# Kernel tuning notes

Hardware: AMD Instinct MI355X
Metric: run time of the kernel (lower is better)

The kernel has to match this reference:

```python
import jax, jax.numpy as jnp
import numpy as np

N = 4096      # num nodes
FIN = 256     # num_in_features
H = 8         # num_of_heads
F = 64        # num_out_features per head
NEG = -1e9    # additive mask value for non-edges


def setup_inputs() -> dict:
    key = jax.random.key(0)
    ks = jax.random.split(key, 7)
    x = jax.random.normal(ks[0], (N, FIN), dtype=jnp.float32)
    adj = jax.random.bernoulli(ks[1], 0.01, (N, N)) | jnp.eye(N, dtype=bool)
    connectivity_mask = jnp.where(adj, 0.0, NEG).astype(jnp.float32)
    # Xavier-uniform-ish scaled params
    W = jax.random.normal(ks[2], (H * F, FIN), dtype=jnp.float32) * np.float32(1.0 / np.sqrt(FIN))
    a_src = jax.random.normal(ks[3], (1, H, F), dtype=jnp.float32) * np.float32(0.1)
    a_tgt = jax.random.normal(ks[4], (1, H, F), dtype=jnp.float32) * np.float32(0.1)
    skip_W = jax.random.normal(ks[5], (H * F, FIN), dtype=jnp.float32) * np.float32(1.0 / np.sqrt(FIN))
    bias = jnp.zeros((H * F,), dtype=jnp.float32)
    return {"x": x, "connectivity_mask": connectivity_mask, "W": W,
            "a_src": a_src, "a_tgt": a_tgt, "skip_W": skip_W, "bias": bias}


def reference(x, connectivity_mask, W, a_src, a_tgt, skip_W, bias):
    # linear_proj (no bias), view to [N, H, F]   (dropout omitted: eval mode)
    proj = (x @ W.T).reshape(N, H, F)
    # per-head scalar scores: [N, H] -> [H, N, 1] and [H, 1, N]
    s_src = jnp.sum(proj * a_src, axis=-1).T[:, :, None]   # [H, N, 1]
    s_tgt = jnp.sum(proj * a_tgt, axis=-1).T[:, None, :]   # [H, 1, N]
    scores = jax.nn.leaky_relu(s_src + s_tgt, negative_slope=0.2)  # [H, N, N]
    alpha = jax.nn.softmax(scores + connectivity_mask[None, :, :], axis=-1)
    # weighted aggregation: bmm(alpha, proj^T) then permute back to [N, H, F]
    out = jnp.einsum('hij,jhf->ihf', alpha, proj)
    # skip connection (dims differ: F_in=256 vs H*F output per head) -> skip_proj
    out = out + (x @ skip_W.T).reshape(N, H, F)
    # concat heads, add bias, ELU activation
    out = out.reshape(N, H * F) + bias
    return jax.nn.elu(out)
```

## Files before the change

### kernel.cpp

```cpp
#include <hip/hip_runtime.h>
#include <hip/hip_bf16.h>

#define NN 4096
#define FIN 256
#define NH 8
#define NF 64
#define HF 512
#define MAXD 128

typedef __attribute__((ext_vector_type(4))) float f32x4;
typedef __attribute__((ext_vector_type(8))) short short8;
typedef unsigned short u16;
typedef unsigned int u32;

union Frag { uint4 u; short8 s; };

__device__ __forceinline__ u16 f2bf(float x) {
    u32 u = __float_as_uint(x);
    u += 0x7fffu + ((u >> 16) & 1u);
    return (u16)(u >> 16);
}
__device__ __forceinline__ float bf2f(u32 lo16) {
    return __uint_as_float(lo16 << 16);
}

__global__ __launch_bounds__(256) void cvt_kernel(
    const float* __restrict__ x, const float* __restrict__ W,
    const float* __restrict__ skW,
    u16* __restrict__ xh, u16* __restrict__ Wh, u16* __restrict__ skWh)
{
    const int gid = blockIdx.x * 256 + threadIdx.x;
    const float* src; u16* dst; int off;
    if (gid < 131072)      { src = x;   dst = xh;   off = gid; }
    else if (gid < 147456) { src = W;   dst = Wh;   off = gid - 131072; }
    else                   { src = skW; dst = skWh; off = gid - 147456; }
    const int e = off * 8;
    const float4 a = *(const float4*)&src[e];
    const float4 b = *(const float4*)&src[e + 4];
    union { u16 h[8]; uint4 v; } pk;
    pk.h[0]=f2bf(a.x); pk.h[1]=f2bf(a.y); pk.h[2]=f2bf(a.z); pk.h[3]=f2bf(a.w);
    pk.h[4]=f2bf(b.x); pk.h[5]=f2bf(b.y); pk.h[6]=f2bf(b.z); pk.h[7]=f2bf(b.w);
    *(uint4*)&dst[e] = pk.v;
}

__global__ __launch_bounds__(256) void gemm_mfma(
    const u16* __restrict__ xh, const u16* __restrict__ Wh,
    const u16* __restrict__ skWh,
    u16* __restrict__ projh, float* __restrict__ skipv)
{
    const int z = blockIdx.z;
    const u16* Bg = z ? skWh : Wh;
    const int bm = blockIdx.y * 128, bn = blockIdx.x * 128;
    __shared__ u16 lds[2][2][8192];
    const int t = threadIdx.x;
    const int w = t >> 6, lane = t & 63;
    const int wm = w >> 1, wn = w & 1;
    const int l15 = lane & 15, lk = lane >> 4;

    f32x4 acc[4][4] = {};

    auto stage = [&](int buf, int ks) {
        const int k0 = ks * 64;
        #pragma unroll
        for (int q = 0; q < 4; ++q) {
            const int s = q * 256 + t;
            const int kk = s >> 9, fr = (s >> 6) & 7;
            const int row = bm + fr * 16 + l15;
            const int kel = k0 + kk * 32 + lk * 8;
            u16* ldst = &lds[buf][0][(q * 256 + w * 64) * 8];
            __builtin_amdgcn_global_load_lds(
                (const __attribute__((address_space(1))) u32*)&xh[row * FIN + kel],
                (__attribute__((address_space(3))) u32*)ldst, 16, 0, 0);
        }
        #pragma unroll
        for (int q = 0; q < 4; ++q) {
            const int s = q * 256 + t;
            const int kk = s >> 9, fr = (s >> 6) & 7;
            const int row = bn + fr * 16 + l15;
            const int kel = k0 + kk * 32 + lk * 8;
            u16* ldst = &lds[buf][1][(q * 256 + w * 64) * 8];
            __builtin_amdgcn_global_load_lds(
                (const __attribute__((address_space(1))) u32*)&Bg[row * FIN + kel],
                (__attribute__((address_space(3))) u32*)ldst, 16, 0, 0);
        }
    };
    auto compute = [&](int buf) {
        const uint4* Ab = (const uint4*)&lds[buf][0][0];
        const uint4* Bb = (const uint4*)&lds[buf][1][0];
        #pragma unroll
        for (int kk = 0; kk < 2; ++kk) {
            Frag a[4], b[4];
            #pragma unroll
            for (int m = 0; m < 4; ++m) a[m].u = Ab[(kk * 8 + wm * 4 + m) * 64 + lane];
            #pragma unroll
            for (int n = 0; n < 4; ++n) b[n].u = Bb[(kk * 8 + wn * 4 + n) * 64 + lane];
            #pragma unroll
            for (int m = 0; m < 4; ++m)
                #pragma unroll
                for (int n = 0; n < 4; ++n)
                    acc[m][n] = __builtin_amdgcn_mfma_f32_16x16x32_bf16(
                        a[m].s, b[n].s, acc[m][n], 0, 0, 0);
        }
    };

    stage(0, 0);
    asm volatile("s_waitcnt vmcnt(0)" ::: "memory");
    __syncthreads();
    int buf = 0;
    for (int ks = 0; ks < 4; ++ks) {
        if (ks < 3) stage(buf ^ 1, ks + 1);
        compute(buf);
        asm volatile("s_waitcnt vmcnt(0)" ::: "memory");
        __syncthreads();
        buf ^= 1;
    }

    #pragma unroll
    for (int m = 0; m < 4; ++m) {
        const int r0 = bm + wm * 64 + m * 16 + lk * 4;
        #pragma unroll
        for (int n = 0; n < 4; ++n) {
            const int c = bn + wn * 64 + n * 16 + l15;
            if (z == 0) {
                #pragma unroll
                for (int rr = 0; rr < 4; ++rr)
                    projh[(size_t)(r0 + rr) * HF + c] = f2bf(acc[m][n][rr]);
            } else {
                #pragma unroll
                for (int rr = 0; rr < 4; ++rr)
                    skipv[(size_t)(r0 + rr) * HF + c] = acc[m][n][rr];
            }
        }
    }
}

__global__ __launch_bounds__(256) void s_kernel(
    const u16* __restrict__ projh, const float* __restrict__ a_src,
    const float* __restrict__ a_tgt, float* __restrict__ s_src,
    float* __restrict__ s_tgt)
{
    const int wg = (blockIdx.x * 256 + threadIdx.x) >> 6;
    const int lane = threadIdx.x & 63;
    const int i = wg >> 3, h = wg & 7;
    const float v = bf2f(projh[(size_t)i * HF + h * NF + lane]);
    float ps = v * a_src[h * NF + lane];
    float pt = v * a_tgt[h * NF + lane];
    #pragma unroll
    for (int off = 32; off; off >>= 1) {
        ps += __shfl_xor(ps, off);
        pt += __shfl_xor(pt, off);
    }
    if (lane == 0) { s_src[h * NN + i] = ps; s_tgt[h * NN + i] = pt; }
}

__global__ __launch_bounds__(256) void scan_kernel(
    const float* __restrict__ mask, int* __restrict__ cnt_g,
    int* __restrict__ nbr_g)
{
    const int i = blockIdx.x, t = threadIdx.x;
    __shared__ int nbr_s[MAXD];
    __shared__ int cnt_s;
    if (t == 0) cnt_s = 0;
    __syncthreads();
    const float4* mrow = (const float4*)&mask[(size_t)i * NN];
    #pragma unroll
    for (int it = 0; it < 4; ++it) {
        const float4 v = mrow[it * 256 + t];
        const int j0 = (it * 256 + t) * 4;
        if (v.x > -0.5f) { int p = atomicAdd(&cnt_s, 1); if (p < MAXD) nbr_s[p] = j0; }
        if (v.y > -0.5f) { int p = atomicAdd(&cnt_s, 1); if (p < MAXD) nbr_s[p] = j0 + 1; }
        if (v.z > -0.5f) { int p = atomicAdd(&cnt_s, 1); if (p < MAXD) nbr_s[p] = j0 + 2; }
        if (v.w > -0.5f) { int p = atomicAdd(&cnt_s, 1); if (p < MAXD) nbr_s[p] = j0 + 3; }
    }
    __syncthreads();
    const int cnt = min(cnt_s, MAXD);
    if (t == 0) cnt_g[i] = cnt;
    if (t < cnt) nbr_g[i * MAXD + t] = nbr_s[t];
}

__global__ __launch_bounds__(256) void agg_kernel(
    const u16* __restrict__ projh, const int* __restrict__ cnt_g,
    const int* __restrict__ nbr_g,
    const float* __restrict__ s_src, const float* __restrict__ s_tgt,
    const float* __restrict__ skipv, const float* __restrict__ bias,
    float* __restrict__ out)
{
    const int i = blockIdx.x, t = threadIdx.x;
    __shared__ int nbr_s[MAXD + 8];
    __shared__ float alpha_s[NH][MAXD + 8];
    __shared__ int cnt_sh;
    if (t == 0) cnt_sh = cnt_g[i];
    __syncthreads();
    const int cnt = cnt_sh;
    if (t < cnt) nbr_s[t] = nbr_g[i * MAXD + t];
    if (t < 8) nbr_s[cnt + t] = i;
    __syncthreads();

    {
        const int h = t >> 5, l = t & 31;
        const float ss = s_src[h * NN + i];
        float sc[4]; float m = -1e30f;
        #pragma unroll
        for (int q = 0; q < 4; ++q) {
            const int k = l + 32 * q;
            if (k < cnt) {
                float s = ss + s_tgt[h * NN + nbr_s[k]];
                s = s > 0.f ? s : 0.2f * s;
                sc[q] = s; m = fmaxf(m, s);
            } else sc[q] = -1e30f;
        }
        #pragma unroll
        for (int off = 16; off; off >>= 1) m = fmaxf(m, __shfl_xor(m, off));
        float p[4]; float psum = 0.f;
        #pragma unroll
        for (int q = 0; q < 4; ++q) {
            p[q] = exp2f((sc[q] - m) * 1.4426950408889634f);
            psum += p[q];
        }
        #pragma unroll
        for (int off = 16; off; off >>= 1) psum += __shfl_xor(psum, off);
        const float inv = 1.0f / psum;
        #pragma unroll
        for (int q = 0; q < 4; ++q) {
            const int k = l + 32 * q;
            if (k < cnt) alpha_s[h][k] = p[q] * inv;
        }
        if (l < 8) alpha_s[h][cnt + l] = 0.f;
    }
    __syncthreads();

    const int w = t >> 6, lane = t & 63;
    const int c = w * 128 + lane * 2;
    const int head = c >> 6, cidx = c >> 1;
    const u32* ph = (const u32*)projh;
    float acc0 = 0.f, acc1 = 0.f;
    const int kmax = (cnt + 7) & ~7;
    for (int k0 = 0; k0 < kmax; k0 += 8) {
        u32 v[8]; float av[8];
        #pragma unroll
        for (int u = 0; u < 8; ++u) {
            v[u] = ph[(size_t)nbr_s[k0 + u] * 256 + cidx];
            av[u] = alpha_s[head][k0 + u];
        }
        #pragma unroll
        for (int u = 0; u < 8; ++u) {
            acc0 += av[u] * bf2f(v[u] & 0xffffu);
            acc1 += av[u] * __uint_as_float(v[u] & 0xffff0000u);
        }
    }

    const float2 sk = *(const float2*)&skipv[(size_t)i * HF + c];
    const float2 bs = *(const float2*)&bias[c];
    float o0 = acc0 + sk.x + bs.x;
    float o1 = acc1 + sk.y + bs.y;
    o0 = o0 > 0.f ? o0 : expm1f(o0);
    o1 = o1 > 0.f ? o1 : expm1f(o1);
    *(float2*)&out[(size_t)i * HF + c] = make_float2(o0, o1);
}

extern "C" void kernel_launch(void* const* d_in, const int* in_sizes, int n_in,
                              void* d_out, int out_size, void* d_ws, size_t ws_size,
                              hipStream_t stream)
{
    (void)in_sizes; (void)n_in; (void)out_size; (void)ws_size;
    const float* x     = (const float*)d_in[0];
    const float* mask  = (const float*)d_in[1];
    const float* W     = (const float*)d_in[2];
    const float* a_src = (const float*)d_in[3];
    const float* a_tgt = (const float*)d_in[4];
    const float* skW   = (const float*)d_in[5];
    const float* bias  = (const float*)d_in[6];
    float* out = (float*)d_out;

    char* ws = (char*)d_ws;
    u16*   xh    = (u16*)(ws);
    u16*   Wh    = (u16*)(ws + 0x200000);
    u16*   skWh  = (u16*)(ws + 0x240000);
    u16*   projh = (u16*)(ws + 0x400000);
    float* skipv = (float*)(ws + 0x800000);
    float* s_src = (float*)(ws + 0x1000000);
    float* s_tgt = (float*)(ws + 0x1020000);
    int*   cnt_g = (int*)(ws + 0x1040000);
    int*   nbr_g = (int*)(ws + 0x1048000);

    scan_kernel<<<dim3(4096), 256, 0, stream>>>(mask, cnt_g, nbr_g);
    cvt_kernel<<<dim3(640), 256, 0, stream>>>(x, W, skW, xh, Wh, skWh);
    gemm_mfma<<<dim3(4, 32, 2), 256, 0, stream>>>(xh, Wh, skWh, projh, skipv);
    s_kernel<<<dim3(8192), 256, 0, stream>>>(projh, a_src, a_tgt, s_src, s_tgt);
    agg_kernel<<<dim3(4096), 256, 0, stream>>>(projh, cnt_g, nbr_g,
                                               s_src, s_tgt, skipv, bias, out);
}
```

Baseline: 145.4 us.

## Fuse scan with bf16 conversion and attention scores into GEMM epilogue

Merges the mask-scan and fp32-to-bf16 conversion kernels into one launch by splitting block ranges, and computes per-head source and target scores inside the projection GEMM epilogue from fp32 accumulators instead of a separate pass over bf16 proj. The score arrays are transposed to node-major layout so agg reads the 8 head scores per node contiguously. This removes two kernel launches and one full reread of proj. The scores now come from unrounded fp32 accumulators, so values change slightly.

```diff
diff --git a/kernel.cpp b/kernel.cpp
--- a/kernel.cpp
+++ b/kernel.cpp
@@ -24,29 +24,56 @@
     return __uint_as_float(lo16 << 16);
 }
 
-__global__ __launch_bounds__(256) void cvt_kernel(
+__global__ __launch_bounds__(256) void scan_cvt(
+    const float* __restrict__ mask, int* __restrict__ cnt_g,
+    int* __restrict__ nbr_g,
     const float* __restrict__ x, const float* __restrict__ W,
     const float* __restrict__ skW,
     u16* __restrict__ xh, u16* __restrict__ Wh, u16* __restrict__ skWh)
 {
-    const int gid = blockIdx.x * 256 + threadIdx.x;
-    const float* src; u16* dst; int off;
-    if (gid < 131072)      { src = x;   dst = xh;   off = gid; }
-    else if (gid < 147456) { src = W;   dst = Wh;   off = gid - 131072; }
-    else                   { src = skW; dst = skWh; off = gid - 147456; }
-    const int e = off * 8;
-    const float4 a = *(const float4*)&src[e];
-    const float4 b = *(const float4*)&src[e + 4];
-    union { u16 h[8]; uint4 v; } pk;
-    pk.h[0]=f2bf(a.x); pk.h[1]=f2bf(a.y); pk.h[2]=f2bf(a.z); pk.h[3]=f2bf(a.w);
-    pk.h[4]=f2bf(b.x); pk.h[5]=f2bf(b.y); pk.h[6]=f2bf(b.z); pk.h[7]=f2bf(b.w);
-    *(uint4*)&dst[e] = pk.v;
-}
-
-__global__ __launch_bounds__(256) void gemm_mfma(
+    const int t = threadIdx.x;
+    if (blockIdx.x >= 4096) {
+        const int gid = (blockIdx.x - 4096) * 256 + t;
+        const float* src; u16* dst; int off;
+        if (gid < 131072)      { src = x;   dst = xh;   off = gid; }
+        else if (gid < 147456) { src = W;   dst = Wh;   off = gid - 131072; }
+        else                   { src = skW; dst = skWh; off = gid - 147456; }
+        const int e = off * 8;
+        const float4 a = *(const float4*)&src[e];
+        const float4 b = *(const float4*)&src[e + 4];
+        union { u16 h[8]; uint4 v; } pk;
+        pk.h[0]=f2bf(a.x); pk.h[1]=f2bf(a.y); pk.h[2]=f2bf(a.z); pk.h[3]=f2bf(a.w);
+        pk.h[4]=f2bf(b.x); pk.h[5]=f2bf(b.y); pk.h[6]=f2bf(b.z); pk.h[7]=f2bf(b.w);
+        *(uint4*)&dst[e] = pk.v;
+        return;
+    }
+    const int i = blockIdx.x;
+    __shared__ int nbr_s[MAXD];
+    __shared__ int cnt_s;
+    if (t == 0) cnt_s = 0;
+    __syncthreads();
+    const float4* mrow = (const float4*)&mask[(size_t)i * NN];
+    #pragma unroll
+    for (int it = 0; it < 4; ++it) {
+        const float4 v = mrow[it * 256 + t];
+        const int j0 = (it * 256 + t) * 4;
+        if (v.x > -0.5f) { int p = atomicAdd(&cnt_s, 1); if (p < MAXD) nbr_s[p] = j0; }
+        if (v.y > -0.5f) { int p = atomicAdd(&cnt_s, 1); if (p < MAXD) nbr_s[p] = j0 + 1; }
+        if (v.z > -0.5f) { int p = atomicAdd(&cnt_s, 1); if (p < MAXD) nbr_s[p] = j0 + 2; }
+        if (v.w > -0.5f) { int p = atomicAdd(&cnt_s, 1); if (p < MAXD) nbr_s[p] = j0 + 3; }
+    }
+    __syncthreads();
+    const int cnt = min(cnt_s, MAXD);
+    if (t == 0) cnt_g[i] = cnt;
+    if (t < cnt) nbr_g[i * MAXD + t] = nbr_s[t];
+}
+
+__global__ __launch_bounds__(256) void gemm_s(
     const u16* __restrict__ xh, const u16* __restrict__ Wh,
     const u16* __restrict__ skWh,
-    u16* __restrict__ projh, float* __restrict__ skipv)
+    const float* __restrict__ a_src, const float* __restrict__ a_tgt,
+    u16* __restrict__ projh, float* __restrict__ skipv,
+    float* __restrict__ s_srcT, float* __restrict__ s_tgtT)
 {
     const int z = blockIdx.z;
     const u16* Bg = z ? skWh : Wh;
@@ -115,17 +142,54 @@
         buf ^= 1;
     }
 
-    #pragma unroll
-    for (int m = 0; m < 4; ++m) {
-        const int r0 = bm + wm * 64 + m * 16 + lk * 4;
-        #pragma unroll
-        for (int n = 0; n < 4; ++n) {
-            const int c = bn + wn * 64 + n * 16 + l15;
-            if (z == 0) {
+    if (z == 0) {
+        #pragma unroll
+        for (int m = 0; m < 4; ++m) {
+            const int r0 = bm + wm * 64 + m * 16 + lk * 4;
+            #pragma unroll
+            for (int n = 0; n < 4; ++n) {
+                const int c = bn + wn * 64 + n * 16 + l15;
                 #pragma unroll
                 for (int rr = 0; rr < 4; ++rr)
                     projh[(size_t)(r0 + rr) * HF + c] = f2bf(acc[m][n][rr]);
-            } else {
+            }
+        }
+        const int h = blockIdx.x * 2 + wn;
+        float as[4], at[4];
+        #pragma unroll
+        for (int n = 0; n < 4; ++n) {
+            as[n] = a_src[h * NF + n * 16 + l15];
+            at[n] = a_tgt[h * NF + n * 16 + l15];
+        }
+        #pragma unroll
+        for (int m = 0; m < 4; ++m) {
+            #pragma unroll
+            for (int rr = 0; rr < 4; ++rr) {
+                float ps = 0.f, pt = 0.f;
+                #pragma unroll
+                for (int n = 0; n < 4; ++n) {
+                    ps += acc[m][n][rr] * as[n];
+                    pt += acc[m][n][rr] * at[n];
+                }
+                #pragma unroll
+                for (int off = 8; off; off >>= 1) {
+                    ps += __shfl_xor(ps, off);
+                    pt += __shfl_xor(pt, off);
+                }
+                if (l15 == 0) {
+                    const int row = bm + wm * 64 + m * 16 + lk * 4 + rr;
+                    s_srcT[row * NH + h] = ps;
+                    s_tgtT[row * NH + h] = pt;
+                }
+            }
+        }
+    } else {
+        #pragma unroll
+        for (int m = 0; m < 4; ++m) {
+            const int r0 = bm + wm * 64 + m * 16 + lk * 4;
+            #pragma unroll
+            for (int n = 0; n < 4; ++n) {
+                const int c = bn + wn * 64 + n * 16 + l15;
                 #pragma unroll
                 for (int rr = 0; rr < 4; ++rr)
                     skipv[(size_t)(r0 + rr) * HF + c] = acc[m][n][rr];
@@ -134,54 +198,10 @@
     }
 }
 
-__global__ __launch_bounds__(256) void s_kernel(
-    const u16* __restrict__ projh, const float* __restrict__ a_src,
-    const float* __restrict__ a_tgt, float* __restrict__ s_src,
-    float* __restrict__ s_tgt)
-{
-    const int wg = (blockIdx.x * 256 + threadIdx.x) >> 6;
-    const int lane = threadIdx.x & 63;
-    const int i = wg >> 3, h = wg & 7;
-    const float v = bf2f(projh[(size_t)i * HF + h * NF + lane]);
-    float ps = v * a_src[h * NF + lane];
-    float pt = v * a_tgt[h * NF + lane];
-    #pragma unroll
-    for (int off = 32; off; off >>= 1) {
-        ps += __shfl_xor(ps, off);
-        pt += __shfl_xor(pt, off);
-    }
-    if (lane == 0) { s_src[h * NN + i] = ps; s_tgt[h * NN + i] = pt; }
-}
-
-__global__ __launch_bounds__(256) void scan_kernel(
-    const float* __restrict__ mask, int* __restrict__ cnt_g,
-    int* __restrict__ nbr_g)
-{
-    const int i = blockIdx.x, t = threadIdx.x;
-    __shared__ int nbr_s[MAXD];
-    __shared__ int cnt_s;
-    if (t == 0) cnt_s = 0;
-    __syncthreads();
-    const float4* mrow = (const float4*)&mask[(size_t)i * NN];
-    #pragma unroll
-    for (int it = 0; it < 4; ++it) {
-        const float4 v = mrow[it * 256 + t];
-        const int j0 = (it * 256 + t) * 4;
-        if (v.x > -0.5f) { int p = atomicAdd(&cnt_s, 1); if (p < MAXD) nbr_s[p] = j0; }
-        if (v.y > -0.5f) { int p = atomicAdd(&cnt_s, 1); if (p < MAXD) nbr_s[p] = j0 + 1; }
-        if (v.z > -0.5f) { int p = atomicAdd(&cnt_s, 1); if (p < MAXD) nbr_s[p] = j0 + 2; }
-        if (v.w > -0.5f) { int p = atomicAdd(&cnt_s, 1); if (p < MAXD) nbr_s[p] = j0 + 3; }
-    }
-    __syncthreads();
-    const int cnt = min(cnt_s, MAXD);
-    if (t == 0) cnt_g[i] = cnt;
-    if (t < cnt) nbr_g[i * MAXD + t] = nbr_s[t];
-}
-
 __global__ __launch_bounds__(256) void agg_kernel(
     const u16* __restrict__ projh, const int* __restrict__ cnt_g,
     const int* __restrict__ nbr_g,
-    const float* __restrict__ s_src, const float* __restrict__ s_tgt,
+    const float* __restrict__ s_srcT, const float* __restrict__ s_tgtT,
     const float* __restrict__ skipv, const float* __restrict__ bias,
     float* __restrict__ out)
 {
@@ -198,13 +218,13 @@
 
     {
         const int h = t >> 5, l = t & 31;
-        const float ss = s_src[h * NN + i];
+        const float ss = s_srcT[i * NH + h];
         float sc[4]; float m = -1e30f;
         #pragma unroll
         for (int q = 0; q < 4; ++q) {
             const int k = l + 32 * q;
             if (k < cnt) {
-                float s = ss + s_tgt[h * NN + nbr_s[k]];
+                float s = ss + s_tgtT[nbr_s[k] * NH + h];
                 s = s > 0.f ? s : 0.2f * s;
                 sc[q] = s; m = fmaxf(m, s);
             } else sc[q] = -1e30f;
@@ -273,20 +293,20 @@
     float* out = (float*)d_out;
 
     char* ws = (char*)d_ws;
-    u16*   xh    = (u16*)(ws);
-    u16*   Wh    = (u16*)(ws + 0x200000);
-    u16*   skWh  = (u16*)(ws + 0x240000);
-    u16*   projh = (u16*)(ws + 0x400000);
-    float* skipv = (float*)(ws + 0x800000);
-    float* s_src = (float*)(ws + 0x1000000);
-    float* s_tgt = (float*)(ws + 0x1020000);
-    int*   cnt_g = (int*)(ws + 0x1040000);
-    int*   nbr_g = (int*)(ws + 0x1048000);
-
-    scan_kernel<<<dim3(4096), 256, 0, stream>>>(mask, cnt_g, nbr_g);
-    cvt_kernel<<<dim3(640), 256, 0, stream>>>(x, W, skW, xh, Wh, skWh);
-    gemm_mfma<<<dim3(4, 32, 2), 256, 0, stream>>>(xh, Wh, skWh, projh, skipv);
-    s_kernel<<<dim3(8192), 256, 0, stream>>>(projh, a_src, a_tgt, s_src, s_tgt);
+    u16*   xh     = (u16*)(ws);
+    u16*   Wh     = (u16*)(ws + 0x200000);
+    u16*   skWh   = (u16*)(ws + 0x240000);
+    u16*   projh  = (u16*)(ws + 0x400000);
+    float* skipv  = (float*)(ws + 0x800000);
+    float* s_srcT = (float*)(ws + 0x1000000);
+    float* s_tgtT = (float*)(ws + 0x1020000);
+    int*   cnt_g  = (int*)(ws + 0x1040000);
+    int*   nbr_g  = (int*)(ws + 0x1048000);
+
+    scan_cvt<<<dim3(4736), 256, 0, stream>>>(mask, cnt_g, nbr_g,
+                                             x, W, skW, xh, Wh, skWh);
+    gemm_s<<<dim3(4, 32, 2), 256, 0, stream>>>(xh, Wh, skWh, a_src, a_tgt,
+                                               projh, skipv, s_srcT, s_tgtT);
     agg_kernel<<<dim3(4096), 256, 0, stream>>>(projh, cnt_g, nbr_g,
-                                               s_src, s_tgt, skipv, bias, out);
-}
+                                               s_srcT, s_tgtT, skipv, bias, out);
+}
```

New measurement: 139.3 us. -4.2%, faster.
